# Performance work log

Measured on AMD Instinct MI355X. Metric: run time of the kernel, lower is better.

## Reference

```python
import jax, jax.numpy as jnp
import numpy as np

E = 16          # n_routed_experts
Z = 8           # zero_expert_num
K = 4           # moe_topk
H = 1024        # hidden_size
I = 768         # moe_intermediate_size
T = 2048        # tokens
SCALE = 2.5     # routed_scaling_factor


def setup_inputs() -> dict:
    key = jax.random.key(0)
    ks = jax.random.split(key, 6)
    return {
        "hidden_states": jax.random.normal(ks[0], (T, H), dtype=jnp.float32),
        "num_global_tokens": T,
        "max_num_tokens_per_gpu": T,
        "w_router": jax.random.normal(ks[1], (E + Z, H), dtype=jnp.float32) * 0.02,
        "correction_bias": jnp.zeros((E + Z,), dtype=jnp.float32),
        "wg": jax.random.normal(ks[2], (E, I, H), dtype=jnp.float32) * 0.02,
        "wu": jax.random.normal(ks[3], (E, I, H), dtype=jnp.float32) * 0.02,
        "wd": jax.random.normal(ks[4], (E, H, I), dtype=jnp.float32) * 0.02,
    }


def reference(hidden_states, num_global_tokens, max_num_tokens_per_gpu,
              w_router, correction_bias, wg, wu, wd):
    x = hidden_states
    # ---- router gemm (always fp32) ----
    logits = x.astype(jnp.float32) @ w_router.T                      # [T, E+Z]
    # ---- DeepSeekV3-style top-k: sigmoid scores, bias only for selection ----
    scores = jax.nn.sigmoid(logits)
    _, topk_ids = jax.lax.top_k(scores + correction_bias[None, :], K)  # [T, K]
    w = jnp.take_along_axis(scores, topk_ids, axis=-1)               # [T, K]
    w = w / jnp.sum(w, axis=-1, keepdims=True)                       # renormalize
    w = w * SCALE                                                    # routed_scaling_factor
    # ---- zero-expert masking (identity type) ----
    zero_mask = topk_ids >= E                                        # [T, K]
    zero_w = jnp.sum(jnp.where(zero_mask, w, 0.0), axis=-1, keepdims=True)
    ids = jnp.where(zero_mask, 0, topk_ids)
    w = jnp.where(zero_mask, 0.0, w)
    # ---- combine weights per (token, expert); masked slots add 0.0 ----
    cw = jnp.zeros((x.shape[0], E), dtype=jnp.float32)
    cw = cw.at[jnp.arange(x.shape[0])[:, None], ids].add(w)          # [T, E]
    # ---- grouped silu-gated expert MLPs (dense compute + masked combine) ----
    g = jnp.einsum('th,eih->eti', x, wg)                             # [E, T, I]
    u = jnp.einsum('th,eih->eti', x, wu)
    a = jax.nn.silu(g) * u
    y = jnp.einsum('eti,ehi->eth', a, wd)                            # [E, T, H]
    routed = jnp.einsum('eth,te->th', y, cw)                         # [T, H]
    return routed + x * zero_w.astype(x.dtype)
```

## Files before the change

### kernel.cpp

```cpp
#include <hip/hip_runtime.h>
#include <hip/hip_bf16.h>
#include <math.h>

typedef __bf16 bf16x8 __attribute__((ext_vector_type(8)));
typedef float f32x4 __attribute__((ext_vector_type(4)));

#define T_TOK 2048
#define HD 1024
#define ID 768
#define NE 16
#define NEZ 24
#define NK 4
#define SCALE_F 2.5f

#define MFMA(a, b, c) __builtin_amdgcn_mfma_f32_16x16x32_bf16(a, b, c, 0, 0, 0)

__device__ __forceinline__ unsigned short f2bf(float f) {
  unsigned int u = __builtin_bit_cast(unsigned int, f);
  u += 0x7FFFu + ((u >> 16) & 1u);
  return (unsigned short)(u >> 16);
}

__device__ __forceinline__ bf16x8 cvt8(float4 a, float4 b) {
  bf16x8 t;
  t[0] = (__bf16)a.x; t[1] = (__bf16)a.y; t[2] = (__bf16)a.z; t[3] = (__bf16)a.w;
  t[4] = (__bf16)b.x; t[5] = (__bf16)b.y; t[6] = (__bf16)b.z; t[7] = (__bf16)b.w;
  return t;
}

__device__ __forceinline__ void gload16(const void* g, void* l) {
  __builtin_amdgcn_global_load_lds(
      (const __attribute__((address_space(1))) void*)(unsigned long long)(uintptr_t)g,
      (__attribute__((address_space(3))) void*)(uintptr_t)l, 16, 0, 0);
}

__global__ __launch_bounds__(256) void router_k(
    const float* __restrict__ x, const float* __restrict__ wr,
    const float* __restrict__ bias,
    int* __restrict__ counts, int* __restrict__ lists, float* __restrict__ wlist,
    unsigned short* __restrict__ xb, float* __restrict__ out) {
  const int wave = threadIdx.x >> 6, l = threadIdx.x & 63;
  const int t = blockIdx.x * 4 + wave;

  float4 xr[4];
#pragma unroll
  for (int c = 0; c < 4; ++c)
    xr[c] = *(const float4*)(x + (size_t)t * HD + c * 256 + l * 4);
#pragma unroll
  for (int c = 0; c < 4; ++c) {
    ushort4 h;
    h.x = f2bf(xr[c].x); h.y = f2bf(xr[c].y); h.z = f2bf(xr[c].z); h.w = f2bf(xr[c].w);
    *(ushort4*)(xb + (size_t)t * HD + c * 256 + l * 4) = h;
  }

  float acc[NEZ];
#pragma unroll 4
  for (int e = 0; e < NEZ; ++e) {
    float4 s = {0.f, 0.f, 0.f, 0.f};
#pragma unroll
    for (int c = 0; c < 4; ++c) {
      float4 w4 = *(const float4*)(wr + (size_t)e * HD + c * 256 + l * 4);
      s.x = fmaf(w4.x, xr[c].x, s.x); s.y = fmaf(w4.y, xr[c].y, s.y);
      s.z = fmaf(w4.z, xr[c].z, s.z); s.w = fmaf(w4.w, xr[c].w, s.w);
    }
    acc[e] = (s.x + s.y) + (s.z + s.w);
  }
#pragma unroll
  for (int s = 1; s < 64; s <<= 1) {
#pragma unroll
    for (int e = 0; e < NEZ; ++e) acc[e] += __shfl_xor(acc[e], s);
  }
  float sc[NEZ], scb[NEZ];
#pragma unroll
  for (int e = 0; e < NEZ; ++e) {
    float s = 1.f / (1.f + expf(-acc[e]));
    sc[e] = s;
    scb[e] = s + bias[e];
  }
  unsigned picked = 0;
  int ids[NK]; float wv[NK]; float ssum = 0.f;
#pragma unroll
  for (int k = 0; k < NK; ++k) {
    int best = 0; float bv = -1e30f; float bsc = 0.f;
#pragma unroll
    for (int e = 0; e < NEZ; ++e) {
      bool take = (((picked >> e) & 1u) == 0) && (scb[e] > bv);
      best = take ? e : best;
      bv = take ? scb[e] : bv;
      bsc = take ? sc[e] : bsc;
    }
    picked |= 1u << best;
    ids[k] = best; wv[k] = bsc; ssum += bsc;
  }
  const float inv = SCALE_F / ssum;
  float zw = 0.f;
#pragma unroll
  for (int k = 0; k < NK; ++k)
    zw += (ids[k] >= NE) ? wv[k] * inv : 0.f;
  if (l < NK) {
    int id = ids[l];
    if (id < NE) {
      int p = atomicAdd(&counts[id], 1);
      lists[id * T_TOK + p] = t;
      wlist[id * T_TOK + p] = wv[l] * inv;
    }
  }
#pragma unroll
  for (int c = 0; c < 4; ++c) {
    float4 o;
    o.x = xr[c].x * zw; o.y = xr[c].y * zw;
    o.z = xr[c].z * zw; o.w = xr[c].w * zw;
    *(float4*)(out + (size_t)t * HD + c * 256 + l * 4) = o;
  }
}

__global__ void scan_k(const int* __restrict__ counts, int* __restrict__ offs) {
  if (threadIdx.x == 0 && blockIdx.x == 0) {
    int s = 0;
    for (int e = 0; e < NE; ++e) { offs[e] = s; s += counts[e]; }
    offs[NE] = s;
  }
}

__global__ __launch_bounds__(256, 3) void gu_k(
    const unsigned short* __restrict__ xb,
    const float* __restrict__ wg, const float* __restrict__ wu,
    const int* __restrict__ counts, const int* __restrict__ offs,
    const int* __restrict__ lists, unsigned short* __restrict__ abuf) {
  const int b = blockIdx.x;
  const int L = (b & 7) * 384 + (b >> 3);
  const int e = L / 192;
  const int rem = L % 192;
  const int xs = rem / 16, ys = rem % 16;
  const int cnt = counts[e];
  const int m0 = ys * 128;
  if (m0 >= cnt) return;
  const int n0 = xs * 64;

  __shared__ int toks[128];
  __shared__ char lds[2][24576];

  const int tid = threadIdx.x;
  if (tid < 128) {
    int m = m0 + tid;
    toks[tid] = (m < cnt) ? lists[e * T_TOK + m] : 0;
  }
  __syncthreads();

  const unsigned short* asrc[2];
#pragma unroll
  for (int j = 0; j < 2; ++j) {
    int row = j * 64 + (tid >> 2);
    int c = ((tid & 3) - (row >> 1)) & 3;
    asrc[j] = xb + (size_t)toks[row] * HD + c * 8;
  }
  const size_t wbase = (size_t)e * ID * HD;
  const float* gsrc[2]; const float* usrc[2];
#pragma unroll
  for (int j = 0; j < 2; ++j) {
    int row = j * 32 + (tid >> 3);
    int c = ((tid & 7) - row) & 7;
    size_t ro = wbase + (size_t)(n0 + row) * HD + c * 4;
    gsrc[j] = wg + ro; usrc[j] = wu + ro;
  }

  const int wid = tid >> 6, l = tid & 63;
  const int wm = (wid >> 1) * 64, wn = (wid & 1) * 32;
  const int q = l >> 4, r = l & 15;

  f32x4 ag[4][2] = {}; f32x4 au[4][2] = {};

  auto stage = [&](int bb, int k0) {
    char* dst = &lds[bb][0] + tid * 16;
#pragma unroll
    for (int j = 0; j < 2; ++j) {
      gload16(asrc[j] + k0, dst + j * 4096);
      gload16(gsrc[j] + k0, dst + 8192 + j * 4096);
      gload16(usrc[j] + k0, dst + 16384 + j * 4096);
    }
  };
  auto comp = [&](int bb) {
    const char* base = &lds[bb][0];
    bf16x8 a[4];
#pragma unroll
    for (int fm = 0; fm < 4; ++fm) {
      int rr = wm + fm * 16 + r;
      int p = (q + (rr >> 1)) & 3;
      a[fm] = *(const bf16x8*)(base + rr * 64 + p * 16);
    }
#pragma unroll
    for (int fn = 0; fn < 2; ++fn) {
      int cc = wn + fn * 16 + r;
      int p0 = (2 * q + cc) & 7, p1 = (2 * q + 1 + cc) & 7;
      const char* pg = base + 8192 + cc * 128;
      const char* pu = base + 16384 + cc * 128;
      float4 g0 = *(const float4*)(pg + p0 * 16);
      float4 g1 = *(const float4*)(pg + p1 * 16);
      float4 u0 = *(const float4*)(pu + p0 * 16);
      float4 u1 = *(const float4*)(pu + p1 * 16);
      bf16x8 bg = cvt8(g0, g1), bu = cvt8(u0, u1);
#pragma unroll
      for (int fm = 0; fm < 4; ++fm) {
        ag[fm][fn] = MFMA(a[fm], bg, ag[fm][fn]);
        au[fm][fn] = MFMA(a[fm], bu, au[fm][fn]);
      }
    }
  };

  stage(0, 0);
  __syncthreads();
  for (int t = 0; t < 32; t += 2) {
    stage(1, (t + 1) * 32);
    comp(0);
    __syncthreads();
    if (t + 2 < 32) stage(0, (t + 2) * 32);
    comp(1);
    __syncthreads();
  }

  const int rowbase = offs[e] + m0;
#pragma unroll
  for (int fm = 0; fm < 4; ++fm)
#pragma unroll
    for (int fn = 0; fn < 2; ++fn)
#pragma unroll
      for (int i2 = 0; i2 < 4; ++i2) {
        int mr = wm + fm * 16 + q * 4 + i2;
        if (m0 + mr < cnt) {
          float g = ag[fm][fn][i2], u = au[fm][fn][i2];
          float s = 1.0f / (1.0f + expf(-g));
          float aa = g * s * u;
          int col = n0 + wn + fn * 16 + r;
          abuf[(size_t)(rowbase + mr) * ID + col] = f2bf(aa);
        }
      }
}

__global__ __launch_bounds__(256, 3) void dn_k(
    const unsigned short* __restrict__ abuf,
    const float* __restrict__ wd,
    const int* __restrict__ counts, const int* __restrict__ offs,
    const int* __restrict__ lists, const float* __restrict__ wlist,
    float* __restrict__ out) {
  const int b = blockIdx.x;
  const int L = (b & 7) * 256 + (b >> 3);
  const int e = L / 128;
  const int rem = L % 128;
  const int xs = rem / 16, ys = rem % 16;
  const int cnt = counts[e];
  const int m0 = ys * 128;
  if (m0 >= cnt) return;
  const int n0 = xs * 128;

  __shared__ int toks[128];
  __shared__ float wts[128];
  __shared__ char lds[2][24576];

  const int tid = threadIdx.x;
  if (tid < 128) {
    int m = m0 + tid;
    if (m < cnt) { toks[tid] = lists[e * T_TOK + m]; wts[tid] = wlist[e * T_TOK + m]; }
    else         { toks[tid] = 0;                    wts[tid] = 0.f; }
  }
  __syncthreads();

  const int rowbase = offs[e] + m0;
  const unsigned short* asrc[2];
#pragma unroll
  for (int j = 0; j < 2; ++j) {
    int row = j * 64 + (tid >> 2);
    int c = ((tid & 3) - (row >> 1)) & 3;
    int grow = (m0 + row < cnt) ? rowbase + row : rowbase;
    asrc[j] = abuf + (size_t)grow * ID + c * 8;
  }
  const float* bsrc[4];
#pragma unroll
  for (int j = 0; j < 4; ++j) {
    int row = j * 32 + (tid >> 3);
    int c = ((tid & 7) - row) & 7;
    bsrc[j] = wd + (size_t)e * HD * ID + (size_t)(n0 + row) * ID + c * 4;
  }

  const int wid = tid >> 6, l = tid & 63;
  const int wm = (wid >> 1) * 64, wn = (wid & 1) * 64;
  const int q = l >> 4, r = l & 15;

  f32x4 acc[4][4] = {};

  auto stage = [&](int bb, int k0) {
    char* dst = &lds[bb][0] + tid * 16;
#pragma unroll
    for (int j = 0; j < 2; ++j) gload16(asrc[j] + k0, dst + j * 4096);
#pragma unroll
    for (int j = 0; j < 4; ++j) gload16(bsrc[j] + k0, dst + 8192 + j * 4096);
  };
  auto comp = [&](int bb) {
    const char* base = &lds[bb][0];
    bf16x8 a[4];
#pragma unroll
    for (int fm = 0; fm < 4; ++fm) {
      int rr = wm + fm * 16 + r;
      int p = (q + (rr >> 1)) & 3;
      a[fm] = *(const bf16x8*)(base + rr * 64 + p * 16);
    }
#pragma unroll
    for (int fn = 0; fn < 4; ++fn) {
      int cc = wn + fn * 16 + r;
      int p0 = (2 * q + cc) & 7, p1 = (2 * q + 1 + cc) & 7;
      const char* pb = base + 8192 + cc * 128;
      float4 b0 = *(const float4*)(pb + p0 * 16);
      float4 b1 = *(const float4*)(pb + p1 * 16);
      bf16x8 bb2 = cvt8(b0, b1);
#pragma unroll
      for (int fm = 0; fm < 4; ++fm)
        acc[fm][fn] = MFMA(a[fm], bb2, acc[fm][fn]);
    }
  };

  stage(0, 0);
  __syncthreads();
  for (int t = 0; t < 24; t += 2) {
    stage(1, (t + 1) * 32);
    comp(0);
    __syncthreads();
    if (t + 2 < 24) stage(0, (t + 2) * 32);
    comp(1);
    __syncthreads();
  }

#pragma unroll
  for (int fm = 0; fm < 4; ++fm)
#pragma unroll
    for (int fn = 0; fn < 4; ++fn)
#pragma unroll
      for (int i2 = 0; i2 < 4; ++i2) {
        int mr = wm + fm * 16 + q * 4 + i2;
        if (m0 + mr < cnt) {
          int col = n0 + wn + fn * 16 + r;
          atomicAdd(&out[(size_t)toks[mr] * HD + col], acc[fm][fn][i2] * wts[mr]);
        }
      }
}

extern "C" void kernel_launch(void* const* d_in, const int* in_sizes, int n_in,
                              void* d_out, int out_size, void* d_ws, size_t ws_size,
                              hipStream_t stream) {
  (void)in_sizes; (void)n_in; (void)out_size; (void)ws_size;
  const float* x    = (const float*)d_in[0];
  const float* wr   = (const float*)d_in[3];
  const float* bias = (const float*)d_in[4];
  const float* wg   = (const float*)d_in[5];
  const float* wu   = (const float*)d_in[6];
  const float* wd   = (const float*)d_in[7];
  float* out = (float*)d_out;

  char* p = (char*)d_ws;
  auto alloc = [&](size_t bytes) {
    char* r = p;
    p += (bytes + 255) & ~(size_t)255;
    return r;
  };
  int*   counts  = (int*)alloc(NE * 4);
  int*   offs    = (int*)alloc((NE + 1) * 4);
  int*   lists   = (int*)alloc((size_t)NE * T_TOK * 4);
  float* wlist   = (float*)alloc((size_t)NE * T_TOK * 4);
  unsigned short* xb   = (unsigned short*)alloc((size_t)T_TOK * HD * 2);
  unsigned short* abuf = (unsigned short*)alloc((size_t)(T_TOK * NK + 128) * ID * 2);

  hipMemsetAsync(counts, 0, NE * 4, stream);
  router_k<<<T_TOK / 4, 256, 0, stream>>>(x, wr, bias, counts, lists, wlist, xb, out);
  scan_k<<<1, 64, 0, stream>>>(counts, offs);
  gu_k<<<3072, 256, 0, stream>>>(xb, wg, wu, counts, offs, lists, abuf);
  dn_k<<<2048, 256, 0, stream>>>(abuf, wd, counts, offs, lists, wlist, out);
}
```

Measured before the change: 128.7 us.

## Triple-buffer LDS staging in expert GEMMs with partial vmcnt waits

Both expert GEMM kernels move from a double-buffered LDS pipeline to three buffers. Each iteration waits with s_waitcnt vmcnt(6) so only the oldest stage must have landed, then issues a single barrier before prefetching two tiles ahead. This puts more global-load latency behind MFMA work and removes one barrier per k-step. In exchange, LDS use grows to 72KB per block and launch bounds drop from 3 to 2 blocks per CU, so occupancy falls.

```diff
diff --git a/kernel.cpp b/kernel.cpp
--- a/kernel.cpp
+++ b/kernel.cpp
@@ -14,6 +14,9 @@
 #define SCALE_F 2.5f
 
 #define MFMA(a, b, c) __builtin_amdgcn_mfma_f32_16x16x32_bf16(a, b, c, 0, 0, 0)
+#define ASM_VMCNT6() asm volatile("s_waitcnt vmcnt(6)" ::: "memory")
+#define ASM_VMCNT0() asm volatile("s_waitcnt vmcnt(0)" ::: "memory")
+#define ASM_BAR()    asm volatile("s_barrier" ::: "memory")
 
 __device__ __forceinline__ unsigned short f2bf(float f) {
   unsigned int u = __builtin_bit_cast(unsigned int, f);
@@ -122,7 +125,7 @@
   }
 }
 
-__global__ __launch_bounds__(256, 3) void gu_k(
+__global__ __launch_bounds__(256, 2) void gu_k(
     const unsigned short* __restrict__ xb,
     const float* __restrict__ wg, const float* __restrict__ wu,
     const int* __restrict__ counts, const int* __restrict__ offs,
@@ -138,7 +141,7 @@
   const int n0 = xs * 64;
 
   __shared__ int toks[128];
-  __shared__ char lds[2][24576];
+  __shared__ char lds3[3 * 24576];
 
   const int tid = threadIdx.x;
   if (tid < 128) {
@@ -171,7 +174,7 @@
   f32x4 ag[4][2] = {}; f32x4 au[4][2] = {};
 
   auto stage = [&](int bb, int k0) {
-    char* dst = &lds[bb][0] + tid * 16;
+    char* dst = lds3 + bb * 24576 + tid * 16;
 #pragma unroll
     for (int j = 0; j < 2; ++j) {
       gload16(asrc[j] + k0, dst + j * 4096);
@@ -180,7 +183,7 @@
     }
   };
   auto comp = [&](int bb) {
-    const char* base = &lds[bb][0];
+    const char* base = lds3 + bb * 24576;
     bf16x8 a[4];
 #pragma unroll
     for (int fm = 0; fm < 4; ++fm) {
@@ -208,15 +211,18 @@
   };
 
   stage(0, 0);
-  __syncthreads();
-  for (int t = 0; t < 32; t += 2) {
-    stage(1, (t + 1) * 32);
-    comp(0);
-    __syncthreads();
-    if (t + 2 < 32) stage(0, (t + 2) * 32);
-    comp(1);
-    __syncthreads();
-  }
+  stage(1, 32);
+  int bi = 0;
+  for (int t = 0; t < 31; ++t) {
+    ASM_VMCNT6();
+    ASM_BAR();
+    if (t <= 29) stage((bi + 2) % 3, (t + 2) * 32);
+    comp(bi);
+    bi = (bi == 2) ? 0 : bi + 1;
+  }
+  ASM_VMCNT0();
+  ASM_BAR();
+  comp(bi);
 
   const int rowbase = offs[e] + m0;
 #pragma unroll
@@ -236,7 +242,7 @@
       }
 }
 
-__global__ __launch_bounds__(256, 3) void dn_k(
+__global__ __launch_bounds__(256, 2) void dn_k(
     const unsigned short* __restrict__ abuf,
     const float* __restrict__ wd,
     const int* __restrict__ counts, const int* __restrict__ offs,
@@ -254,7 +260,7 @@
 
   __shared__ int toks[128];
   __shared__ float wts[128];
-  __shared__ char lds[2][24576];
+  __shared__ char lds3[3 * 24576];
 
   const int tid = threadIdx.x;
   if (tid < 128) {
@@ -288,14 +294,14 @@
   f32x4 acc[4][4] = {};
 
   auto stage = [&](int bb, int k0) {
-    char* dst = &lds[bb][0] + tid * 16;
+    char* dst = lds3 + bb * 24576 + tid * 16;
 #pragma unroll
     for (int j = 0; j < 2; ++j) gload16(asrc[j] + k0, dst + j * 4096);
 #pragma unroll
     for (int j = 0; j < 4; ++j) gload16(bsrc[j] + k0, dst + 8192 + j * 4096);
   };
   auto comp = [&](int bb) {
-    const char* base = &lds[bb][0];
+    const char* base = lds3 + bb * 24576;
     bf16x8 a[4];
 #pragma unroll
     for (int fm = 0; fm < 4; ++fm) {
@@ -318,15 +324,18 @@
   };
 
   stage(0, 0);
-  __syncthreads();
-  for (int t = 0; t < 24; t += 2) {
-    stage(1, (t + 1) * 32);
-    comp(0);
-    __syncthreads();
-    if (t + 2 < 24) stage(0, (t + 2) * 32);
-    comp(1);
-    __syncthreads();
-  }
+  stage(1, 32);
+  int bi = 0;
+  for (int t = 0; t < 23; ++t) {
+    ASM_VMCNT6();
+    ASM_BAR();
+    if (t <= 21) stage((bi + 2) % 3, (t + 2) * 32);
+    comp(bi);
+    bi = (bi == 2) ? 0 : bi + 1;
+  }
+  ASM_VMCNT0();
+  ASM_BAR();
+  comp(bi);
 
 #pragma unroll
   for (int fm = 0; fm < 4; ++fm)
```

Result: slower. 152.1 us (+18.2%).

## Double M tile to 256 rows with 512-thread blocks in expert GEMMs

Applied to the files above, without the earlier changes.

Both expert GEMM kernels now use 512-thread blocks covering 256 token rows instead of 128, so each staged fp32 weight tile is reused across twice as many tokens. This halves weight reloads from global memory and the per-block fp32-to-bf16 conversion overhead. The shared token/weight index arrays and their barrier are dropped in favour of direct per-thread lookups from the lists. The trade-off is more tail waste for experts whose token counts are not multiples of 256, fewer blocks in flight, and higher register and LDS pressure under the new launch bounds.

```diff
diff --git a/kernel.cpp b/kernel.cpp
--- a/kernel.cpp
+++ b/kernel.cpp
@@ -122,46 +122,42 @@
   }
 }
 
-__global__ __launch_bounds__(256, 3) void gu_k(
+__global__ __launch_bounds__(512, 4) void gu_k(
     const unsigned short* __restrict__ xb,
     const float* __restrict__ wg, const float* __restrict__ wu,
     const int* __restrict__ counts, const int* __restrict__ offs,
     const int* __restrict__ lists, unsigned short* __restrict__ abuf) {
   const int b = blockIdx.x;
-  const int L = (b & 7) * 384 + (b >> 3);
-  const int e = L / 192;
-  const int rem = L % 192;
-  const int xs = rem / 16, ys = rem % 16;
+  const int L = (b & 7) * 192 + (b >> 3);
+  const int e = L / 96;
+  const int rem = L % 96;
+  const int xs = rem / 8, ys = rem % 8;
   const int cnt = counts[e];
-  const int m0 = ys * 128;
+  const int m0 = ys * 256;
   if (m0 >= cnt) return;
   const int n0 = xs * 64;
 
-  __shared__ int toks[128];
-  __shared__ char lds[2][24576];
+  __shared__ char lds[2][32768];
 
   const int tid = threadIdx.x;
-  if (tid < 128) {
-    int m = m0 + tid;
-    toks[tid] = (m < cnt) ? lists[e * T_TOK + m] : 0;
-  }
-  __syncthreads();
 
   const unsigned short* asrc[2];
 #pragma unroll
   for (int j = 0; j < 2; ++j) {
-    int row = j * 64 + (tid >> 2);
-    int c = ((tid & 3) - (row >> 1)) & 3;
-    asrc[j] = xb + (size_t)toks[row] * HD + c * 8;
+    int u = j * 512 + tid;
+    int row = u >> 2;
+    int m = m0 + row; if (m >= cnt) m = cnt - 1;
+    int tok = lists[e * T_TOK + m];
+    int c = ((u & 3) - (row >> 1)) & 3;
+    asrc[j] = xb + (size_t)tok * HD + c * 8;
   }
   const size_t wbase = (size_t)e * ID * HD;
-  const float* gsrc[2]; const float* usrc[2];
-#pragma unroll
-  for (int j = 0; j < 2; ++j) {
-    int row = j * 32 + (tid >> 3);
+  const float* gsrc; const float* usrc;
+  {
+    int row = tid >> 3;
     int c = ((tid & 7) - row) & 7;
     size_t ro = wbase + (size_t)(n0 + row) * HD + c * 4;
-    gsrc[j] = wg + ro; usrc[j] = wu + ro;
+    gsrc = wg + ro; usrc = wu + ro;
   }
 
   const int wid = tid >> 6, l = tid & 63;
@@ -171,13 +167,12 @@
   f32x4 ag[4][2] = {}; f32x4 au[4][2] = {};
 
   auto stage = [&](int bb, int k0) {
-    char* dst = &lds[bb][0] + tid * 16;
-#pragma unroll
-    for (int j = 0; j < 2; ++j) {
-      gload16(asrc[j] + k0, dst + j * 4096);
-      gload16(gsrc[j] + k0, dst + 8192 + j * 4096);
-      gload16(usrc[j] + k0, dst + 16384 + j * 4096);
-    }
+    char* base = &lds[bb][0];
+#pragma unroll
+    for (int j = 0; j < 2; ++j)
+      gload16(asrc[j] + k0, base + (j * 512 + tid) * 16);
+    gload16(gsrc + k0, base + 16384 + tid * 16);
+    gload16(usrc + k0, base + 24576 + tid * 16);
   };
   auto comp = [&](int bb) {
     const char* base = &lds[bb][0];
@@ -192,8 +187,8 @@
     for (int fn = 0; fn < 2; ++fn) {
       int cc = wn + fn * 16 + r;
       int p0 = (2 * q + cc) & 7, p1 = (2 * q + 1 + cc) & 7;
-      const char* pg = base + 8192 + cc * 128;
-      const char* pu = base + 16384 + cc * 128;
+      const char* pg = base + 16384 + cc * 128;
+      const char* pu = base + 24576 + cc * 128;
       float4 g0 = *(const float4*)(pg + p0 * 16);
       float4 g1 = *(const float4*)(pg + p1 * 16);
       float4 u0 = *(const float4*)(pu + p0 * 16);
@@ -236,48 +231,42 @@
       }
 }
 
-__global__ __launch_bounds__(256, 3) void dn_k(
+__global__ __launch_bounds__(512, 4) void dn_k(
     const unsigned short* __restrict__ abuf,
     const float* __restrict__ wd,
     const int* __restrict__ counts, const int* __restrict__ offs,
     const int* __restrict__ lists, const float* __restrict__ wlist,
     float* __restrict__ out) {
   const int b = blockIdx.x;
-  const int L = (b & 7) * 256 + (b >> 3);
-  const int e = L / 128;
-  const int rem = L % 128;
-  const int xs = rem / 16, ys = rem % 16;
+  const int L = (b & 7) * 128 + (b >> 3);
+  const int e = L / 64;
+  const int rem = L % 64;
+  const int xs = rem / 8, ys = rem % 8;
   const int cnt = counts[e];
-  const int m0 = ys * 128;
+  const int m0 = ys * 256;
   if (m0 >= cnt) return;
   const int n0 = xs * 128;
 
-  __shared__ int toks[128];
-  __shared__ float wts[128];
-  __shared__ char lds[2][24576];
+  __shared__ char lds[2][32768];
 
   const int tid = threadIdx.x;
-  if (tid < 128) {
-    int m = m0 + tid;
-    if (m < cnt) { toks[tid] = lists[e * T_TOK + m]; wts[tid] = wlist[e * T_TOK + m]; }
-    else         { toks[tid] = 0;                    wts[tid] = 0.f; }
-  }
-  __syncthreads();
-
   const int rowbase = offs[e] + m0;
+
   const unsigned short* asrc[2];
 #pragma unroll
   for (int j = 0; j < 2; ++j) {
-    int row = j * 64 + (tid >> 2);
-    int c = ((tid & 3) - (row >> 1)) & 3;
-    int grow = (m0 + row < cnt) ? rowbase + row : rowbase;
-    asrc[j] = abuf + (size_t)grow * ID + c * 8;
-  }
-  const float* bsrc[4];
-#pragma unroll
-  for (int j = 0; j < 4; ++j) {
-    int row = j * 32 + (tid >> 3);
-    int c = ((tid & 7) - row) & 7;
+    int u = j * 512 + tid;
+    int row = u >> 2;
+    int m = m0 + row; if (m >= cnt) m = cnt - 1;
+    int c = ((u & 3) - (row >> 1)) & 3;
+    asrc[j] = abuf + (size_t)(offs[e] + m) * ID + c * 8;
+  }
+  const float* bsrc[2];
+#pragma unroll
+  for (int j = 0; j < 2; ++j) {
+    int u = j * 512 + tid;
+    int row = u >> 3;
+    int c = ((u & 7) - row) & 7;
     bsrc[j] = wd + (size_t)e * HD * ID + (size_t)(n0 + row) * ID + c * 4;
   }
 
@@ -288,11 +277,12 @@
   f32x4 acc[4][4] = {};
 
   auto stage = [&](int bb, int k0) {
-    char* dst = &lds[bb][0] + tid * 16;
-#pragma unroll
-    for (int j = 0; j < 2; ++j) gload16(asrc[j] + k0, dst + j * 4096);
-#pragma unroll
-    for (int j = 0; j < 4; ++j) gload16(bsrc[j] + k0, dst + 8192 + j * 4096);
+    char* base = &lds[bb][0];
+#pragma unroll
+    for (int j = 0; j < 2; ++j) {
+      gload16(asrc[j] + k0, base + (j * 512 + tid) * 16);
+      gload16(bsrc[j] + k0, base + 16384 + (j * 512 + tid) * 16);
+    }
   };
   auto comp = [&](int bb) {
     const char* base = &lds[bb][0];
@@ -307,7 +297,7 @@
     for (int fn = 0; fn < 4; ++fn) {
       int cc = wn + fn * 16 + r;
       int p0 = (2 * q + cc) & 7, p1 = (2 * q + 1 + cc) & 7;
-      const char* pb = base + 8192 + cc * 128;
+      const char* pb = base + 16384 + cc * 128;
       float4 b0 = *(const float4*)(pb + p0 * 16);
       float4 b1 = *(const float4*)(pb + p1 * 16);
       bf16x8 bb2 = cvt8(b0, b1);
@@ -329,17 +319,21 @@
   }
 
 #pragma unroll
-  for (int fm = 0; fm < 4; ++fm)
-#pragma unroll
-    for (int fn = 0; fn < 4; ++fn)
-#pragma unroll
-      for (int i2 = 0; i2 < 4; ++i2) {
-        int mr = wm + fm * 16 + q * 4 + i2;
-        if (m0 + mr < cnt) {
+  for (int fm = 0; fm < 4; ++fm) {
+#pragma unroll
+    for (int i2 = 0; i2 < 4; ++i2) {
+      int mr = wm + fm * 16 + q * 4 + i2;
+      if (m0 + mr < cnt) {
+        int tok = lists[e * T_TOK + m0 + mr];
+        float wt = wlist[e * T_TOK + m0 + mr];
+#pragma unroll
+        for (int fn = 0; fn < 4; ++fn) {
           int col = n0 + wn + fn * 16 + r;
-          atomicAdd(&out[(size_t)toks[mr] * HD + col], acc[fm][fn][i2] * wts[mr]);
+          atomicAdd(&out[(size_t)tok * HD + col], acc[fm][fn][i2] * wt);
         }
       }
+    }
+  }
 }
 
 extern "C" void kernel_launch(void* const* d_in, const int* in_sizes, int n_in,
@@ -365,11 +359,11 @@
   int*   lists   = (int*)alloc((size_t)NE * T_TOK * 4);
   float* wlist   = (float*)alloc((size_t)NE * T_TOK * 4);
   unsigned short* xb   = (unsigned short*)alloc((size_t)T_TOK * HD * 2);
-  unsigned short* abuf = (unsigned short*)alloc((size_t)(T_TOK * NK + 128) * ID * 2);
+  unsigned short* abuf = (unsigned short*)alloc((size_t)(T_TOK * NK + 256) * ID * 2);
 
   hipMemsetAsync(counts, 0, NE * 4, stream);
   router_k<<<T_TOK / 4, 256, 0, stream>>>(x, wr, bias, counts, lists, wlist, xb, out);
   scan_k<<<1, 64, 0, stream>>>(counts, offs);
-  gu_k<<<3072, 256, 0, stream>>>(xb, wg, wu, counts, offs, lists, abuf);
-  dn_k<<<2048, 256, 0, stream>>>(abuf, wd, counts, offs, lists, wlist, out);
-}
+  gu_k<<<1536, 512, 0, stream>>>(xb, wg, wu, counts, offs, lists, abuf);
+  dn_k<<<1024, 512, 0, stream>>>(abuf, wd, counts, offs, lists, wlist, out);
+}
```

New measurement: 165.0 us. 1.28x slower.

## Replace atomic scatter-add with per-slot bf16 output buffer and combine kernel

Applied to the files above, without the earlier changes.

The down-projection kernel no longer does float atomicAdd into the output. It writes weighted results as bf16 into a per-(token, k) slot buffer, and a new combine kernel sums the four slots plus the zero-expert identity term. The scan kernel is also removed, and each block computes its expert offset by summing counts inline. This trades scattered atomics for an extra 16MB memset, an extra kernel pass, and bf16 rounding of the partial results.

```diff
diff --git a/kernel.cpp b/kernel.cpp
--- a/kernel.cpp
+++ b/kernel.cpp
@@ -20,6 +20,10 @@
   u += 0x7FFFu + ((u >> 16) & 1u);
   return (unsigned short)(u >> 16);
 }
+__device__ __forceinline__ float bf2f(unsigned short h) {
+  unsigned int u = ((unsigned int)h) << 16;
+  return __builtin_bit_cast(float, u);
+}
 
 __device__ __forceinline__ bf16x8 cvt8(float4 a, float4 b) {
   bf16x8 t;
@@ -38,7 +42,8 @@
     const float* __restrict__ x, const float* __restrict__ wr,
     const float* __restrict__ bias,
     int* __restrict__ counts, int* __restrict__ lists, float* __restrict__ wlist,
-    unsigned short* __restrict__ xb, float* __restrict__ out) {
+    int* __restrict__ klist, float* __restrict__ zwv,
+    unsigned short* __restrict__ xb) {
   const int wave = threadIdx.x >> 6, l = threadIdx.x & 63;
   const int t = blockIdx.x * 4 + wave;
 
@@ -97,35 +102,22 @@
 #pragma unroll
   for (int k = 0; k < NK; ++k)
     zw += (ids[k] >= NE) ? wv[k] * inv : 0.f;
+  if (l == 0) zwv[t] = zw;
   if (l < NK) {
     int id = ids[l];
     if (id < NE) {
       int p = atomicAdd(&counts[id], 1);
       lists[id * T_TOK + p] = t;
       wlist[id * T_TOK + p] = wv[l] * inv;
-    }
-  }
-#pragma unroll
-  for (int c = 0; c < 4; ++c) {
-    float4 o;
-    o.x = xr[c].x * zw; o.y = xr[c].y * zw;
-    o.z = xr[c].z * zw; o.w = xr[c].w * zw;
-    *(float4*)(out + (size_t)t * HD + c * 256 + l * 4) = o;
-  }
-}
-
-__global__ void scan_k(const int* __restrict__ counts, int* __restrict__ offs) {
-  if (threadIdx.x == 0 && blockIdx.x == 0) {
-    int s = 0;
-    for (int e = 0; e < NE; ++e) { offs[e] = s; s += counts[e]; }
-    offs[NE] = s;
+      klist[id * T_TOK + p] = t * NK + l;
+    }
   }
 }
 
 __global__ __launch_bounds__(256, 3) void gu_k(
     const unsigned short* __restrict__ xb,
     const float* __restrict__ wg, const float* __restrict__ wu,
-    const int* __restrict__ counts, const int* __restrict__ offs,
+    const int* __restrict__ counts,
     const int* __restrict__ lists, unsigned short* __restrict__ abuf) {
   const int b = blockIdx.x;
   const int L = (b & 7) * 384 + (b >> 3);
@@ -137,6 +129,9 @@
   if (m0 >= cnt) return;
   const int n0 = xs * 64;
 
+  int offs_e = 0;
+  for (int i = 0; i < e; ++i) offs_e += counts[i];
+
   __shared__ int toks[128];
   __shared__ char lds[2][24576];
 
@@ -218,7 +213,7 @@
     __syncthreads();
   }
 
-  const int rowbase = offs[e] + m0;
+  const int rowbase = offs_e + m0;
 #pragma unroll
   for (int fm = 0; fm < 4; ++fm)
 #pragma unroll
@@ -239,9 +234,9 @@
 __global__ __launch_bounds__(256, 3) void dn_k(
     const unsigned short* __restrict__ abuf,
     const float* __restrict__ wd,
-    const int* __restrict__ counts, const int* __restrict__ offs,
-    const int* __restrict__ lists, const float* __restrict__ wlist,
-    float* __restrict__ out) {
+    const int* __restrict__ counts,
+    const int* __restrict__ klist, const float* __restrict__ wlist,
+    unsigned short* __restrict__ ybuf) {
   const int b = blockIdx.x;
   const int L = (b & 7) * 256 + (b >> 3);
   const int e = L / 128;
@@ -252,26 +247,21 @@
   if (m0 >= cnt) return;
   const int n0 = xs * 128;
 
-  __shared__ int toks[128];
-  __shared__ float wts[128];
+  int offs_e = 0;
+  for (int i = 0; i < e; ++i) offs_e += counts[i];
+
   __shared__ char lds[2][24576];
 
   const int tid = threadIdx.x;
-  if (tid < 128) {
-    int m = m0 + tid;
-    if (m < cnt) { toks[tid] = lists[e * T_TOK + m]; wts[tid] = wlist[e * T_TOK + m]; }
-    else         { toks[tid] = 0;                    wts[tid] = 0.f; }
-  }
-  __syncthreads();
-
-  const int rowbase = offs[e] + m0;
+  const int rowbase = offs_e + m0;
+
   const unsigned short* asrc[2];
 #pragma unroll
   for (int j = 0; j < 2; ++j) {
     int row = j * 64 + (tid >> 2);
     int c = ((tid & 3) - (row >> 1)) & 3;
-    int grow = (m0 + row < cnt) ? rowbase + row : rowbase;
-    asrc[j] = abuf + (size_t)grow * ID + c * 8;
+    int m = m0 + row; if (m >= cnt) m = cnt - 1;
+    asrc[j] = abuf + (size_t)(offs_e + m) * ID + c * 8;
   }
   const float* bsrc[4];
 #pragma unroll
@@ -329,17 +319,38 @@
   }
 
 #pragma unroll
-  for (int fm = 0; fm < 4; ++fm)
-#pragma unroll
-    for (int fn = 0; fn < 4; ++fn)
-#pragma unroll
-      for (int i2 = 0; i2 < 4; ++i2) {
-        int mr = wm + fm * 16 + q * 4 + i2;
-        if (m0 + mr < cnt) {
+  for (int fm = 0; fm < 4; ++fm) {
+#pragma unroll
+    for (int i2 = 0; i2 < 4; ++i2) {
+      int mr = wm + fm * 16 + q * 4 + i2;
+      if (m0 + mr < cnt) {
+        int slot = klist[e * T_TOK + m0 + mr];
+        float wt = wlist[e * T_TOK + m0 + mr];
+#pragma unroll
+        for (int fn = 0; fn < 4; ++fn) {
           int col = n0 + wn + fn * 16 + r;
-          atomicAdd(&out[(size_t)toks[mr] * HD + col], acc[fm][fn][i2] * wts[mr]);
+          ybuf[(size_t)slot * HD + col] = f2bf(acc[fm][fn][i2] * wt);
         }
       }
+    }
+  }
+}
+
+__global__ __launch_bounds__(256) void comb_k(
+    const float* __restrict__ x, const float* __restrict__ zwv,
+    const unsigned short* __restrict__ ybuf, float* __restrict__ out) {
+  const int t = blockIdx.x;
+  const int c = threadIdx.x;
+  const float z = zwv[t];
+  float4 xv = *(const float4*)(x + (size_t)t * HD + c * 4);
+  float4 o;
+  o.x = xv.x * z; o.y = xv.y * z; o.z = xv.z * z; o.w = xv.w * z;
+#pragma unroll
+  for (int k = 0; k < NK; ++k) {
+    ushort4 yv = *(const ushort4*)(ybuf + ((size_t)(t * NK + k)) * HD + c * 4);
+    o.x += bf2f(yv.x); o.y += bf2f(yv.y); o.z += bf2f(yv.z); o.w += bf2f(yv.w);
+  }
+  *(float4*)(out + (size_t)t * HD + c * 4) = o;
 }
 
 extern "C" void kernel_launch(void* const* d_in, const int* in_sizes, int n_in,
@@ -361,15 +372,18 @@
     return r;
   };
   int*   counts  = (int*)alloc(NE * 4);
-  int*   offs    = (int*)alloc((NE + 1) * 4);
   int*   lists   = (int*)alloc((size_t)NE * T_TOK * 4);
   float* wlist   = (float*)alloc((size_t)NE * T_TOK * 4);
+  int*   klist   = (int*)alloc((size_t)NE * T_TOK * 4);
+  float* zwv     = (float*)alloc((size_t)T_TOK * 4);
   unsigned short* xb   = (unsigned short*)alloc((size_t)T_TOK * HD * 2);
   unsigned short* abuf = (unsigned short*)alloc((size_t)(T_TOK * NK + 128) * ID * 2);
+  unsigned short* ybuf = (unsigned short*)alloc((size_t)T_TOK * NK * HD * 2);
 
   hipMemsetAsync(counts, 0, NE * 4, stream);
-  router_k<<<T_TOK / 4, 256, 0, stream>>>(x, wr, bias, counts, lists, wlist, xb, out);
-  scan_k<<<1, 64, 0, stream>>>(counts, offs);
-  gu_k<<<3072, 256, 0, stream>>>(xb, wg, wu, counts, offs, lists, abuf);
-  dn_k<<<2048, 256, 0, stream>>>(abuf, wd, counts, offs, lists, wlist, out);
-}
+  hipMemsetAsync(ybuf, 0, (size_t)T_TOK * NK * HD * 2, stream);
+  router_k<<<T_TOK / 4, 256, 0, stream>>>(x, wr, bias, counts, lists, wlist, klist, zwv, xb);
+  gu_k<<<3072, 256, 0, stream>>>(xb, wg, wu, counts, lists, abuf);
+  dn_k<<<2048, 256, 0, stream>>>(abuf, wd, counts, klist, wlist, ybuf);
+  comb_k<<<T_TOK, 256, 0, stream>>>(x, zwv, ybuf, out);
+}
```

Measured after the change: 138.3 us. +7.5%, slower.
